# Performance work log

Measured on AMD Instinct MI355X. Metric: run time of the kernel, lower is better.

The kernel has to match this reference:

```python
import jax, jax.numpy as jnp
import numpy as np

N_EMBD = 1024
N_HEADS = 16
HEAD_DIM = N_EMBD // N_HEADS
T = 1024
B = 1
WINDOW = 64
LM_STRIDE = 64


def _build_neigh_idx(T, window, stride, n_heads, seed):
    """Per-head neighbor index [H, T, D], padded with -1.

    Neighbors of i: cycle prev/next (sorted), causal window i-window..i-1,
    landmarks j%stride==0 with j<i, then self; deduped preserving order.
    Matches _build_neighbors_index with a single random cycle per head.
    """
    rng = np.random.default_rng(seed)
    n_land = (T + stride - 1) // stride
    D = 2 + window + n_land + 1  # max_cycle_deg + window + landmarks + self
    out = np.full((n_heads, T, D), -1, dtype=np.int64)
    lands = list(range(0, T, stride))
    for h in range(n_heads):
        perm = rng.permutation(T)
        inv = np.argsort(perm)
        prev = perm[(inv - 1) % T]
        nxt = perm[(inv + 1) % T]
        for i in range(T):
            neigh = sorted({int(prev[i]), int(nxt[i])})
            neigh += list(range(max(0, i - window), i))
            neigh += [j for j in lands if j < i]
            neigh.append(i)
            seen = set()
            ded = []
            for j in neigh:
                if j not in seen:
                    ded.append(j)
                    seen.add(j)
            out[h, i, :len(ded)] = ded
    return out


def setup_inputs() -> dict:
    key = jax.random.key(0)
    k1, k2, k3 = jax.random.split(key, 3)
    scale = 1.0 / np.sqrt(N_EMBD)
    x = jax.random.normal(k1, (B, T, N_EMBD), dtype=jnp.float32)
    Wqkv = jax.random.normal(k2, (N_EMBD, 3 * N_EMBD), dtype=jnp.float32) * scale
    Wout = jax.random.normal(k3, (N_EMBD, N_EMBD), dtype=jnp.float32) * scale
    neigh_idx = jnp.asarray(_build_neigh_idx(T, WINDOW, LM_STRIDE, N_HEADS, seed=0))
    return {"x": x, "Wqkv": Wqkv, "Wout": Wout, "neigh_idx": neigh_idx}


def reference(x, Wqkv, Wout, neigh_idx):
    Bv, Tv, C = x.shape
    H, dh = N_HEADS, HEAD_DIM
    qkv = x @ Wqkv  # [B,T,3C]
    q, k, v = jnp.split(qkv, 3, axis=-1)
    q = q.reshape(Bv, Tv, H, dh).transpose(0, 2, 1, 3)  # [B,H,T,dh]
    k = k.reshape(Bv, Tv, H, dh).transpose(0, 2, 1, 3)
    v = v.reshape(Bv, Tv, H, dh).transpose(0, 2, 1, 3)

    safe = jnp.clip(neigh_idx, 0)  # [H,T,D]
    h_ix = jnp.arange(H)[:, None, None]
    k_g = k[:, h_ix, safe, :]  # [B,H,T,D,dh]
    v_g = v[:, h_ix, safe, :]

    scores = jnp.einsum("bhtd,bhtnd->bhtn", q, k_g) / np.sqrt(dh)
    valid = neigh_idx >= 0
    causal = safe <= jnp.arange(Tv)[None, :, None]
    mask = valid & causal  # [H,T,D]; self always present -> rows non-empty
    scores = jnp.where(mask[None], scores, -jnp.inf)
    w = jax.nn.softmax(scores, axis=-1)  # [B,H,T,D]
    y = jnp.einsum("bhtn,bhtnd->bhtd", w, v_g)  # [B,H,T,dh]
    y = y.transpose(0, 2, 1, 3).reshape(Bv, Tv, C)
    return y @ Wout
```

## Files before the change

### kernel.cpp

```cpp
#include <hip/hip_runtime.h>
#include <math.h>

#define NH 16
#define TT 1024
#define HD 64
#define NE 1024

typedef unsigned int u32;
typedef unsigned short u16;
typedef __bf16 bf16x8 __attribute__((ext_vector_type(8)));
typedef float f32x4 __attribute__((ext_vector_type(4)));

__device__ inline u16 f2bf(float f) {
  u32 u = __builtin_bit_cast(u32, f);
  u32 r = (u + 0x7fffu + ((u >> 16) & 1u)) >> 16;
  return (u16)r;
}
__device__ inline float bf2f(u16 h) {
  return __builtin_bit_cast(float, (u32)h << 16);
}
__device__ inline void gload16(const void* g, void* l) {
  __builtin_amdgcn_global_load_lds((const __attribute__((address_space(1))) void*)g,
                                   (__attribute__((address_space(3))) void*)l, 16, 0, 0);
}

__global__ __launch_bounds__(256) void prep(const float* __restrict__ x,
                                            const float* __restrict__ Wqkv,
                                            const float* __restrict__ Wout,
                                            u16* __restrict__ xb,
                                            u16* __restrict__ WqkvT,
                                            u16* __restrict__ WoutT) {
  __shared__ float tile[64][65];
  const int tid = threadIdx.x;
  const int bx = blockIdx.x;
  if (bx < 1024) {
    int i = bx * 256 + tid;
    float4 f = ((const float4*)x)[i];
    ushort4 o = {f2bf(f.x), f2bf(f.y), f2bf(f.z), f2bf(f.w)};
    ((ushort4*)xb)[i] = o;
    return;
  }
  int b = bx - 1024;
  int nb = b & 63, kb = b >> 6;
  const float* W; u16* WT; int N, n0;
  if (nb < 48) { W = Wqkv; WT = WqkvT; N = 3 * NE; n0 = nb * 64; }
  else         { W = Wout; WT = WoutT; N = NE;     n0 = (nb - 48) * 64; }
  const int k0 = kb * 64;
#pragma unroll
  for (int it = 0; it < 16; ++it) {
    int idx = it * 256 + tid;
    int r = idx >> 6, c = idx & 63;
    tile[r][c] = W[(size_t)(k0 + r) * N + n0 + c];
  }
  __syncthreads();
#pragma unroll
  for (int it = 0; it < 16; ++it) {
    int idx = it * 256 + tid;
    int nn = idx >> 6, kk = idx & 63;
    WT[(size_t)(n0 + nn) * NE + k0 + kk] = f2bf(tile[kk][nn]);
  }
}

template<int R>
__device__ __forceinline__ void stage_rows(const u16* __restrict__ G, int ldk,
                                           u16* L, int tid) {
#pragma unroll
  for (int it = 0; it < R / 32; ++it) {
    int idx = it * 256 + tid;
    int r = idx >> 3, kg = idx & 7;
    gload16(G + (size_t)r * ldk + ((kg ^ (r & 7)) << 3), L + (idx << 3));
  }
}

template<int MODE, int NT>
__global__ __launch_bounds__(256) void gemm_direct(const u16* __restrict__ A,
                                                   const u16* __restrict__ Bt,
                                                   void* __restrict__ Cv,
                                                   int M, int N, int K) {
  __shared__ u16 As[2][64 * 64];
  __shared__ u16 Bs[2][NT * 64];
  const int tid = threadIdx.x;
  const int lane = tid & 63;
  const int wv = tid >> 6;
  const int wm = wv >> 1, wn = wv & 1;
  const int row0 = blockIdx.y * 64;
  const int col0 = blockIdx.x * NT;
  const int nsteps = K >> 6;
  constexpr int NI = NT / 32;

  const u16* Ab = A + (size_t)row0 * K;
  const u16* Bb = Bt + (size_t)col0 * K;

  f32x4 acc[2][NI] = {};

  stage_rows<64>(Ab, K, As[0], tid);
  stage_rows<NT>(Bb, K, Bs[0], tid);
  __syncthreads();

  int buf = 0;
  for (int ks = 0; ks < nsteps; ++ks) {
    if (ks + 1 < nsteps) {
      stage_rows<64>(Ab + (ks + 1) * 64, K, As[buf ^ 1], tid);
      stage_rows<NT>(Bb + (ks + 1) * 64, K, Bs[buf ^ 1], tid);
    }
#pragma unroll
    for (int half = 0; half < 2; ++half) {
      const int kk = half * 32;
      bf16x8 af[2], bfr[NI];
#pragma unroll
      for (int mi = 0; mi < 2; ++mi) {
        int r = wm * 32 + mi * 16 + (lane & 15);
        int c = (kk >> 3) + (lane >> 4);
        af[mi] = *(const bf16x8*)&As[buf][(r * 8 + (c ^ (r & 7))) * 8];
      }
#pragma unroll
      for (int ni = 0; ni < NI; ++ni) {
        int r = wn * (NT / 2) + ni * 16 + (lane & 15);
        int c = (kk >> 3) + (lane >> 4);
        bfr[ni] = *(const bf16x8*)&Bs[buf][(r * 8 + (c ^ (r & 7))) * 8];
      }
#pragma unroll
      for (int mi = 0; mi < 2; ++mi)
#pragma unroll
        for (int ni = 0; ni < NI; ++ni)
          acc[mi][ni] = __builtin_amdgcn_mfma_f32_16x16x32_bf16(af[mi], bfr[ni], acc[mi][ni], 0, 0, 0);
    }
    __syncthreads();
    buf ^= 1;
  }

  const int rbase = row0 + wm * 32 + (lane >> 4) * 4;
  const int cbase = col0 + wn * (NT / 2) + (lane & 15);
#pragma unroll
  for (int mi = 0; mi < 2; ++mi) {
#pragma unroll
    for (int ni = 0; ni < NI; ++ni) {
      int n = cbase + ni * 16;
#pragma unroll
      for (int r = 0; r < 4; ++r) {
        int t = rbase + mi * 16 + r;
        float val = acc[mi][ni][r];
        if (MODE == 0) {
          ((float*)Cv)[(size_t)t * N + n] = val;
        } else {
          int which = n >> 10, h = (n & 1023) >> 6, d = n & 63;
          ((u16*)Cv)[(size_t)which * (NH * TT * HD) + (size_t)h * (TT * HD) +
                     (size_t)t * HD + d] = f2bf(val);
        }
      }
    }
  }
}

__global__ __launch_bounds__(256) void attn4(const u16* __restrict__ qkv,
                                             const int* __restrict__ nidx,
                                             u16* __restrict__ y, int D) {
  __shared__ __align__(16) u16 Qs[16 * 64];
  __shared__ __align__(16) u16 Ks[128 * 64];
  __shared__ __align__(16) u16 Vt[64 * 128];
  __shared__ int pn_l[32];
  __shared__ int colj[128];
  __shared__ float rinv[16];
  float* S = (float*)Ks;
  u16* P = (u16*)((char*)Ks + 8448);

  const int tid = threadIdx.x;
  const int lane = tid & 63;
  const int wv = tid >> 6;
  const int h = blockIdx.y;
  const int t0 = blockIdx.x * 16;

  const u16* qh = qkv + (size_t)h * TT * HD;
  const u16* kh = qkv + (size_t)NH * TT * HD + (size_t)h * TT * HD;
  const u16* vh = qkv + 2 * (size_t)NH * TT * HD + (size_t)h * TT * HD;

  if (tid < 32) pn_l[tid] = nidx[((size_t)h * TT + t0 + (tid >> 1)) * D + (tid & 1)];
  __syncthreads();

  if (tid < 128) {
    int c = tid, j;
    if (c < 80) {
      j = t0 - 64 + c;
      if (j < 0) j = -1;
    } else if (c < 96) {
      j = (c - 80) * 64;
      if (j >= t0 - 64) j = -1;
    } else {
      int s = c - 96;
      j = pn_l[s];
      bool keep = (j < t0 - 64) && ((j & 63) != 0);
      if (keep)
        for (int s2 = 0; s2 < s; ++s2)
          if (pn_l[s2] == j) { keep = false; break; }
      if (!keep) j = -1;
    }
    colj[c] = j;
  }
  __syncthreads();

  if (tid < 128) {
    int row = tid >> 3, slot = tid & 7, ch = slot ^ (row & 7);
    gload16(qh + (size_t)(t0 + row) * HD + ch * 8, Qs + tid * 8);
  }
  uint4 vreg[4];
#pragma unroll
  for (int it = 0; it < 4; ++it) {
    int idx = it * 256 + tid;
    int col = idx >> 3, slot = idx & 7, ch = slot ^ (col & 7);
    int j = colj[col]; if (j < 0) j = 0;
    gload16(kh + (size_t)j * HD + ch * 8, Ks + idx * 8);
  }
#pragma unroll
  for (int it = 0; it < 4; ++it) {
    int idx = it * 256 + tid;
    int col = idx >> 3, ch = idx & 7;
    int j = colj[col]; if (j < 0) j = 0;
    vreg[it] = *(const uint4*)(vh + (size_t)j * HD + ch * 8);
  }
  __syncthreads();

  f32x4 sc[2] = {};
  bf16x8 af[2];
#pragma unroll
  for (int half = 0; half < 2; ++half) {
    int row = lane & 15;
    int chunk = 4 * half + (lane >> 4);
    af[half] = *(const bf16x8*)&Qs[(row * 8 + (chunk ^ (row & 7))) * 8];
  }
#pragma unroll
  for (int p = 0; p < 2; ++p) {
    int col = 16 * (2 * wv + p) + (lane & 15);
#pragma unroll
    for (int half = 0; half < 2; ++half) {
      int chunk = 4 * half + (lane >> 4);
      bf16x8 bfv = *(const bf16x8*)&Ks[(col * 8 + (chunk ^ (col & 7))) * 8];
      sc[p] = __builtin_amdgcn_mfma_f32_16x16x32_bf16(af[half], bfv, sc[p], 0, 0, 0);
    }
  }
  __syncthreads();

#pragma unroll
  for (int p = 0; p < 2; ++p) {
    int col = 16 * (2 * wv + p) + (lane & 15);
    int j = colj[col];
#pragma unroll
    for (int r = 0; r < 4; ++r) {
      int row = (lane >> 4) * 4 + r;
      int i = t0 + row;
      int p0 = pn_l[2 * row], p1 = pn_l[2 * row + 1];
      bool m;
      if (col < 80)      m = (j >= 0) && (j <= i) &&
                             ((i - j) <= 64 || (j & 63) == 0 || j == p0 || j == p1);
      else if (col < 96) m = (j >= 0);
      else               m = (j >= 0) && (j == p0 || j == p1);
      S[row * 132 + col] = m ? ((float)sc[p][r]) * 0.125f : -1e30f;
    }
  }
  __syncthreads();

  {
    int row = tid >> 4, q = tid & 15;
    float v[8];
    float mx = -3e38f;
#pragma unroll
    for (int e = 0; e < 8; ++e) {
      v[e] = S[row * 132 + 8 * q + e];
      mx = fmaxf(mx, v[e]);
    }
#pragma unroll
    for (int off = 1; off < 16; off <<= 1) mx = fmaxf(mx, __shfl_xor(mx, off, 64));
    float sum = 0.f;
#pragma unroll
    for (int e = 0; e < 8; ++e) {
      v[e] = __expf(v[e] - mx);
      sum += v[e];
    }
#pragma unroll
    for (int off = 1; off < 16; off <<= 1) sum += __shfl_xor(sum, off, 64);
    if (q == 0) rinv[row] = 1.0f / sum;
    u32 w0 = (u32)f2bf(v[0]) | ((u32)f2bf(v[1]) << 16);
    u32 w1 = (u32)f2bf(v[2]) | ((u32)f2bf(v[3]) << 16);
    u32 w2 = (u32)f2bf(v[4]) | ((u32)f2bf(v[5]) << 16);
    u32 w3 = (u32)f2bf(v[6]) | ((u32)f2bf(v[7]) << 16);
    uint4 pk = {w0, w1, w2, w3};
    *(uint4*)&P[row * 128 + ((q ^ (row & 7)) << 3)] = pk;
  }

#pragma unroll
  for (int it = 0; it < 4; ++it) {
    int idx = it * 256 + tid;
    int col = idx >> 3, ch = idx & 7;
    const u32* vw = (const u32*)&vreg[it];
#pragma unroll
    for (int e = 0; e < 8; ++e) {
      int d = ch * 8 + e;
      u16 val = (e & 1) ? (u16)(vw[e >> 1] >> 16) : (u16)(vw[e >> 1] & 0xffffu);
      int swz = (col >> 3) ^ e ^ ch;
      Vt[d * 128 + swz * 8 + (col & 7)] = val;
    }
  }
  __syncthreads();

  f32x4 oacc = {};
#pragma unroll
  for (int ks2 = 0; ks2 < 4; ++ks2) {
    int rowp = lane & 15;
    int chp = ks2 * 4 + (lane >> 4);
    bf16x8 pa = *(const bf16x8*)&P[rowp * 128 + ((chp ^ (rowp & 7)) << 3)];
    int dd = wv * 16 + (lane & 15);
    int swz = chp ^ (dd & 7) ^ ((dd >> 3) & 7);
    bf16x8 vb = *(const bf16x8*)&Vt[dd * 128 + swz * 8];
    oacc = __builtin_amdgcn_mfma_f32_16x16x32_bf16(pa, vb, oacc, 0, 0, 0);
  }
  {
    int dd = wv * 16 + (lane & 15);
#pragma unroll
    for (int r = 0; r < 4; ++r) {
      int row = (lane >> 4) * 4 + r;
      y[(size_t)(t0 + row) * NE + h * HD + dd] = f2bf(oacc[r] * rinv[row]);
    }
  }
}

extern "C" void kernel_launch(void* const* d_in, const int* in_sizes, int n_in,
                              void* d_out, int out_size, void* d_ws, size_t ws_size,
                              hipStream_t stream) {
  const float* x    = (const float*)d_in[0];
  const float* Wqkv = (const float*)d_in[1];
  const float* Wout = (const float*)d_in[2];
  const int*   nidx = (const int*)d_in[3];
  float* out = (float*)d_out;

  u16* ws16  = (u16*)d_ws;
  u16* xb    = ws16;
  u16* WqkvT = ws16 + 1048576;
  u16* WoutT = ws16 + 4194304;
  u16* qkvb  = ws16 + 5242880;

  const int D = in_sizes[3] / (NH * TT);

  prep<<<2048, 256, 0, stream>>>(x, Wqkv, Wout, xb, WqkvT, WoutT);

  gemm_direct<1, 64><<<dim3(48, 16), 256, 0, stream>>>(xb, WqkvT, qkvb, TT, 3 * NE, NE);

  attn4<<<dim3(TT / 16, NH), 256, 0, stream>>>(qkvb, nidx, xb, D);

  gemm_direct<0, 32><<<dim3(32, 16), 256, 0, stream>>>(xb, WoutT, out, TT, NE, NE);
}
```

Measured before the change: 46.46 us.

## Remap block indices per XCD for L2 locality and vectorize V transpose

Both GEMMs and the attention kernel now use a 1-D grid. Block ids are remapped so that blocks landing on the same XCD (bid&7) share weight column tiles or attention heads, which should improve reuse in each XCD's private L2. The Q tile load is issued earlier so it overlaps the neighbor-index setup. The V transpose into LDS is restructured so each thread gathers 4 consecutive columns and writes packed 8-byte stores instead of 32 scalar 2-byte stores. The remapping relies on the hardware dispatching blocks round-robin across the 8 XCDs.

Result: no change. 45.84 us (-1.3%).

```diff
diff --git a/kernel.cpp b/kernel.cpp
--- a/kernel.cpp
+++ b/kernel.cpp
@@ -22,6 +22,10 @@
 __device__ inline void gload16(const void* g, void* l) {
   __builtin_amdgcn_global_load_lds((const __attribute__((address_space(1))) void*)g,
                                    (__attribute__((address_space(3))) void*)l, 16, 0, 0);
+}
+__device__ inline u16 h16(uint4 v, int e) {
+  u32 w = ((const u32*)&v)[e >> 1];
+  return (e & 1) ? (u16)(w >> 16) : (u16)(w & 0xffffu);
 }
 
 __global__ __launch_bounds__(256) void prep(const float* __restrict__ x,
@@ -72,7 +76,7 @@
   }
 }
 
-template<int MODE, int NT>
+template<int MODE, int NT, int CPX>
 __global__ __launch_bounds__(256) void gemm_direct(const u16* __restrict__ A,
                                                    const u16* __restrict__ Bt,
                                                    void* __restrict__ Cv,
@@ -83,8 +87,10 @@
   const int lane = tid & 63;
   const int wv = tid >> 6;
   const int wm = wv >> 1, wn = wv & 1;
-  const int row0 = blockIdx.y * 64;
-  const int col0 = blockIdx.x * NT;
+  const int bid = blockIdx.x;
+  const int xcd = bid & 7, loc = bid >> 3;
+  const int row0 = (loc / CPX) * 64;
+  const int col0 = (xcd * CPX + loc % CPX) * NT;
   const int nsteps = K >> 6;
   constexpr int NI = NT / 32;
 
@@ -152,7 +158,7 @@
   }
 }
 
-__global__ __launch_bounds__(256) void attn4(const u16* __restrict__ qkv,
+__global__ __launch_bounds__(256) void attn5(const u16* __restrict__ qkv,
                                              const int* __restrict__ nidx,
                                              u16* __restrict__ y, int D) {
   __shared__ __align__(16) u16 Qs[16 * 64];
@@ -167,14 +173,20 @@
   const int tid = threadIdx.x;
   const int lane = tid & 63;
   const int wv = tid >> 6;
-  const int h = blockIdx.y;
-  const int t0 = blockIdx.x * 16;
+  const int bid = blockIdx.x;
+  const int xcd = bid & 7, loc = bid >> 3;
+  const int h = xcd * 2 + (loc & 1);
+  const int t0 = (loc >> 1) * 16;
 
   const u16* qh = qkv + (size_t)h * TT * HD;
   const u16* kh = qkv + (size_t)NH * TT * HD + (size_t)h * TT * HD;
   const u16* vh = qkv + 2 * (size_t)NH * TT * HD + (size_t)h * TT * HD;
 
   if (tid < 32) pn_l[tid] = nidx[((size_t)h * TT + t0 + (tid >> 1)) * D + (tid & 1)];
+  if (tid < 128) {
+    int row = tid >> 3, slot = tid & 7, ch = slot ^ (row & 7);
+    gload16(qh + (size_t)(t0 + row) * HD + ch * 8, Qs + tid * 8);
+  }
   __syncthreads();
 
   if (tid < 128) {
@@ -198,11 +210,6 @@
   }
   __syncthreads();
 
-  if (tid < 128) {
-    int row = tid >> 3, slot = tid & 7, ch = slot ^ (row & 7);
-    gload16(qh + (size_t)(t0 + row) * HD + ch * 8, Qs + tid * 8);
-  }
-  uint4 vreg[4];
 #pragma unroll
   for (int it = 0; it < 4; ++it) {
     int idx = it * 256 + tid;
@@ -210,12 +217,14 @@
     int j = colj[col]; if (j < 0) j = 0;
     gload16(kh + (size_t)j * HD + ch * 8, Ks + idx * 8);
   }
+  const int d0 = (tid & 7) * 8;
+  const int cq = tid >> 3;
+  uint4 vreg[4];
 #pragma unroll
   for (int it = 0; it < 4; ++it) {
-    int idx = it * 256 + tid;
-    int col = idx >> 3, ch = idx & 7;
+    int col = cq * 4 + it;
     int j = colj[col]; if (j < 0) j = 0;
-    vreg[it] = *(const uint4*)(vh + (size_t)j * HD + ch * 8);
+    vreg[it] = *(const uint4*)(vh + (size_t)j * HD + d0);
   }
   __syncthreads();
 
@@ -287,17 +296,13 @@
   }
 
 #pragma unroll
-  for (int it = 0; it < 4; ++it) {
-    int idx = it * 256 + tid;
-    int col = idx >> 3, ch = idx & 7;
-    const u32* vw = (const u32*)&vreg[it];
-#pragma unroll
-    for (int e = 0; e < 8; ++e) {
-      int d = ch * 8 + e;
-      u16 val = (e & 1) ? (u16)(vw[e >> 1] >> 16) : (u16)(vw[e >> 1] & 0xffffu);
-      int swz = (col >> 3) ^ e ^ ch;
-      Vt[d * 128 + swz * 8 + (col & 7)] = val;
-    }
+  for (int e = 0; e < 8; ++e) {
+    int d = d0 + e;
+    u32 lo = (u32)h16(vreg[0], e) | ((u32)h16(vreg[1], e) << 16);
+    u32 hi = (u32)h16(vreg[2], e) | ((u32)h16(vreg[3], e) << 16);
+    int oswz = (cq >> 1) ^ (d & 7) ^ ((d >> 3) & 7);
+    uint2 pk2 = {lo, hi};
+    *(uint2*)&Vt[d * 128 + oswz * 8 + (cq & 1) * 4] = pk2;
   }
   __syncthreads();
 
@@ -341,9 +346,9 @@
 
   prep<<<2048, 256, 0, stream>>>(x, Wqkv, Wout, xb, WqkvT, WoutT);
 
-  gemm_direct<1, 64><<<dim3(48, 16), 256, 0, stream>>>(xb, WqkvT, qkvb, TT, 3 * NE, NE);
-
-  attn4<<<dim3(TT / 16, NH), 256, 0, stream>>>(qkvb, nidx, xb, D);
-
-  gemm_direct<0, 32><<<dim3(32, 16), 256, 0, stream>>>(xb, WoutT, out, TT, NE, NE);
-}
+  gemm_direct<1, 64, 6><<<768, 256, 0, stream>>>(xb, WqkvT, qkvb, TT, 3 * NE, NE);
+
+  attn5<<<1024, 256, 0, stream>>>(qkvb, nidx, xb, D);
+
+  gemm_direct<0, 32, 4><<<512, 256, 0, stream>>>(xb, WoutT, out, TT, NE, NE);
+}
```
